# Performance work log

Hardware: AMD Instinct MI355X
Metric: run time of the kernel (lower is better)

## Reference

```python
import jax, jax.numpy as jnp
import numpy as np

V = 4          # view_num
B = 2048       # batch_size
D = 512        # feature dim
N = V * B
TEMP = 0.5     # temperature
EPS = 1e-8     # torch CosineSimilarity eps


def _neg_idx():
    # Row with residue p (position within its view block) masks out columns c
    # with c % B == p (the positive/self positions), exactly matching
    # mask_positive_samples: fill_diagonal_(0) on every BxB block.
    cols = np.arange(N)
    return np.stack([cols[cols % B != p] for p in range(B)])  # [B, N-V]

_NEG_IDX = jnp.asarray(_neg_idx())


def setup_inputs() -> dict:
    key = jax.random.key(0)
    x = jax.random.normal(key, (V, B, D), dtype=jnp.float32)
    return {"x": x}


def reference(x):
    # torch.cat(input, dim=0) -> [N, D]
    xf = x.reshape(N, D)
    # Cosine similarity via normalize + matmul (same math as broadcasted
    # CosineSimilarity(dim=2), expressed efficiently).
    norm = jnp.maximum(jnp.linalg.norm(xf, axis=1, keepdims=True), EPS)
    xn = xf / norm
    sim = (xn @ xn.T) / TEMP                                  # [N, N]

    # Negatives per anchor row: gather masked columns (same column order as
    # torch boolean-mask indexing, which is row-major ascending).
    sim_v = sim.reshape(V, B, N)
    negs = jnp.take_along_axis(sim_v, _NEG_IDX[None], axis=2)  # [V, B, N-V]
    lse_neg = jax.nn.logsumexp(negs, axis=2)                   # [V, B]

    # pos[i, j, b] = sim block-diagonal between views i and j
    pos = jnp.diagonal(sim.reshape(V, B, V, B), axis1=1, axis2=3)  # [V, V, B]

    # CrossEntropy with label 0 on logits = [pos_ij, negatives_i]:
    #   loss_b = logsumexp([pos, negs]) - pos = logaddexp(pos, lse_neg) - pos
    lse = jnp.logaddexp(pos, lse_neg[:, None, :])              # [V, V, B]
    per_pair = (lse - pos).sum(axis=2) / B                     # [V, V]

    off_diag = 1.0 - jnp.eye(V, dtype=per_pair.dtype)          # skip j == i
    return jnp.sum(per_pair * off_diag)
```

## Files before the change

kernel.cpp:

```cpp
#include <hip/hip_runtime.h>

#define NV 4
#define NB 2048
#define ND 512
#define NN 8192

typedef __bf16 bf16x8 __attribute__((ext_vector_type(8)));
typedef float floatx4 __attribute__((ext_vector_type(4)));

__global__ __launch_bounds__(256) void normalize_k(const float* __restrict__ x,
                                                   __bf16* __restrict__ xn,
                                                   float* __restrict__ sumexp,
                                                   float* __restrict__ out) {
  if (threadIdx.x < 4) sumexp[blockIdx.x * 4 + threadIdx.x] = 0.0f;
  if (blockIdx.x == 0 && threadIdx.x == 0) out[0] = 0.0f;

  const int row = blockIdx.x * 4 + (threadIdx.x >> 6);
  const int l = threadIdx.x & 63;
  const float4* xr = (const float4*)(x + (size_t)row * ND);
  float4 v0 = xr[l * 2 + 0];
  float4 v1 = xr[l * 2 + 1];
  float ss = v0.x * v0.x + v0.y * v0.y + v0.z * v0.z + v0.w * v0.w +
             v1.x * v1.x + v1.y * v1.y + v1.z * v1.z + v1.w * v1.w;
#pragma unroll
  for (int off = 32; off > 0; off >>= 1) ss += __shfl_xor(ss, off, 64);
  const float inv = 1.0f / fmaxf(sqrtf(ss), 1e-8f);
  bf16x8 o;
  o[0] = (__bf16)(v0.x * inv); o[1] = (__bf16)(v0.y * inv);
  o[2] = (__bf16)(v0.z * inv); o[3] = (__bf16)(v0.w * inv);
  o[4] = (__bf16)(v1.x * inv); o[5] = (__bf16)(v1.y * inv);
  o[6] = (__bf16)(v1.z * inv); o[7] = (__bf16)(v1.w * inv);
  *(bf16x8*)(xn + (size_t)row * ND + l * 8) = o;
}

__device__ __forceinline__ void gl_lds16(const void* g, void* l) {
  __builtin_amdgcn_global_load_lds(
      (const __attribute__((address_space(1))) void*)g,
      (__attribute__((address_space(3))) void*)l, 16, 0, 0);
}

__global__ __launch_bounds__(256, 4) void sim_k(const __bf16* __restrict__ xn,
                                                float* __restrict__ sumexp,
                                                float* __restrict__ pos) {
  __shared__ __bf16 As[128 * 32];
  __shared__ __bf16 Bs[128 * 32];
  const int tid = threadIdx.x;
  const int w = tid >> 6, l = tid & 63;
  const int m = l & 15, q = l >> 4;
  const int wr = w >> 1, wc = w & 1;

  const int bid = blockIdx.x;
  int rt = (int)((129.0f - sqrtf(16641.0f - 8.0f * (float)bid)) * 0.5f);
  rt = rt < 0 ? 0 : (rt > 63 ? 63 : rt);
  while (rt > 0 && (rt * 64 - rt * (rt - 1) / 2) > bid) --rt;
  while (rt < 63 && ((rt + 1) * 64 - (rt + 1) * rt / 2) <= bid) ++rt;
  const int ct = rt + (bid - (rt * 64 - rt * (rt - 1) / 2));
  const bool diag = (rt == ct);

  floatx4 acc[4][4] = {};

  const char* gA = (const char*)xn + (size_t)rt * 128 * (ND * 2);
  const char* gB = (const char*)xn + (size_t)ct * 128 * (ND * 2);
  char* lA = (char*)As;
  char* lB = (char*)Bs;

  const int row0 = tid >> 2;
  const int kb = (tid & 3) * 16;

  for (int kt = 0; kt < ND / 32; ++kt) {
    const int kbyte0 = kt * 64;
    {
      const char* ga0 = gA + (size_t)row0 * (ND * 2) + kbyte0 + kb;
      const char* gb0 = gB + (size_t)row0 * (ND * 2) + kbyte0 + kb;
      const char* ga1 = gA + (size_t)(row0 + 64) * (ND * 2) + kbyte0 + kb;
      const char* gb1 = gB + (size_t)(row0 + 64) * (ND * 2) + kbyte0 + kb;
      gl_lds16(ga0, lA + w * 1024);
      gl_lds16(gb0, lB + w * 1024);
      gl_lds16(ga1, lA + 4096 + w * 1024);
      gl_lds16(gb1, lB + 4096 + w * 1024);
    }
    __syncthreads();
    bf16x8 af[4], bfr[4];
#pragma unroll
    for (int mt = 0; mt < 4; ++mt)
      af[mt] = *(const bf16x8*)(lA + (wr * 64 + mt * 16 + m) * 64 + q * 16);
#pragma unroll
    for (int nt = 0; nt < 4; ++nt)
      bfr[nt] = *(const bf16x8*)(lB + (wc * 64 + nt * 16 + m) * 64 + q * 16);
#pragma unroll
    for (int mt = 0; mt < 4; ++mt)
#pragma unroll
      for (int nt = 0; nt < 4; ++nt)
        acc[mt][nt] = __builtin_amdgcn_mfma_f32_16x16x32_bf16(
            af[mt], bfr[nt], acc[mt][nt], 0, 0, 0);
    __syncthreads();
  }

  const int r0 = rt * 128 + wr * 64;
  const int c0 = ct * 128 + wc * 64;
  float cs[4] = {0.f, 0.f, 0.f, 0.f};
#pragma unroll
  for (int mt = 0; mt < 4; ++mt) {
    float rs[4] = {0.f, 0.f, 0.f, 0.f};
#pragma unroll
    for (int nt = 0; nt < 4; ++nt) {
      const int c = c0 + nt * 16 + m;
#pragma unroll
      for (int reg = 0; reg < 4; ++reg) {
        const int r = r0 + mt * 16 + q * 4 + reg;
        const float s = acc[mt][nt][reg] * 2.0f;
        if (((c - r) & (NB - 1)) == 0) {
          pos[r * NV + (c >> 11)] = s;
          if (!diag) pos[c * NV + (r >> 11)] = s;
        } else {
          const float e = __expf(s);
          rs[reg] += e;
          cs[nt] += e;
        }
      }
    }
#pragma unroll
    for (int off = 1; off < 16; off <<= 1) {
#pragma unroll
      for (int reg = 0; reg < 4; ++reg) rs[reg] += __shfl_xor(rs[reg], off, 64);
    }
    if (m < 4) atomicAdd(&sumexp[r0 + mt * 16 + q * 4 + m], rs[m]);
  }
  if (!diag) {
#pragma unroll
    for (int nt = 0; nt < 4; ++nt) {
      cs[nt] += __shfl_xor(cs[nt], 16, 64);
      cs[nt] += __shfl_xor(cs[nt], 32, 64);
    }
    if (q == 0) {
#pragma unroll
      for (int nt = 0; nt < 4; ++nt)
        atomicAdd(&sumexp[c0 + nt * 16 + m], cs[nt]);
    }
  }
}

__global__ __launch_bounds__(256) void finalize_k(
    const float* __restrict__ sumexp, const float* __restrict__ pos,
    float* __restrict__ out) {
  const int r = blockIdx.x * 256 + threadIdx.x;
  const float se = sumexp[r];
  const int i = r >> 11;
  float local = 0.0f;
#pragma unroll
  for (int j = 0; j < NV; ++j) {
    if (j == i) continue;
    const float p = pos[r * NV + j];
    local += logf(__expf(p) + se) - p;
  }
  local *= (1.0f / NB);
#pragma unroll
  for (int off = 32; off > 0; off >>= 1) local += __shfl_xor(local, off, 64);
  if ((threadIdx.x & 63) == 0) atomicAdd(out, local);
}

extern "C" void kernel_launch(void* const* d_in, const int* in_sizes, int n_in,
                              void* d_out, int out_size, void* d_ws,
                              size_t ws_size, hipStream_t stream) {
  const float* x = (const float*)d_in[0];
  float* out = (float*)d_out;
  char* ws = (char*)d_ws;
  __bf16* xn = (__bf16*)ws;
  float* sumexp = (float*)(ws + (size_t)NN * ND * 2);
  float* pos = (float*)(ws + (size_t)NN * ND * 2 + NN * 4);

  normalize_k<<<NN / 4, 256, 0, stream>>>(x, xn, sumexp, out);
  sim_k<<<64 * 65 / 2, 256, 0, stream>>>(xn, sumexp, pos);
  finalize_k<<<NN / 256, 256, 0, stream>>>(sumexp, pos, out);
}
```

Baseline: 120.2 us.

## Switch similarity GEMM to FP8 e4m3 with scaled MFMA and swizzled LDS tiles

Normalized features are now quantized to FP8 e4m3 instead of bf16, and the Gram matrix is computed with the MI355X scaled MFMA 16x16x128 f8f6f4 instruction using unit scales. K tiles grow to 128 bytes per row, with an XOR swizzle on the LDS layout to avoid bank conflicts and a fully unrolled 4-step K loop. This halves operand bytes and raises MFMA throughput per instruction, at the cost of lower precision in the similarity values that feed exp and logsumexp. LDS use grows, so occupancy drops to three blocks per CU.

```diff
diff --git a/kernel.cpp b/kernel.cpp
--- a/kernel.cpp
+++ b/kernel.cpp
@@ -1,15 +1,17 @@
 #include <hip/hip_runtime.h>
+#include <hip/hip_fp8.h>
 
 #define NV 4
 #define NB 2048
 #define ND 512
 #define NN 8192
 
-typedef __bf16 bf16x8 __attribute__((ext_vector_type(8)));
+typedef int int8v __attribute__((ext_vector_type(8)));
 typedef float floatx4 __attribute__((ext_vector_type(4)));
+#define SCALE1 0x7F7F7F7Fu
 
 __global__ __launch_bounds__(256) void normalize_k(const float* __restrict__ x,
-                                                   __bf16* __restrict__ xn,
+                                                   unsigned char* __restrict__ xn,
                                                    float* __restrict__ sumexp,
                                                    float* __restrict__ out) {
   if (threadIdx.x < 4) sumexp[blockIdx.x * 4 + threadIdx.x] = 0.0f;
@@ -25,12 +27,16 @@
 #pragma unroll
   for (int off = 32; off > 0; off >>= 1) ss += __shfl_xor(ss, off, 64);
   const float inv = 1.0f / fmaxf(sqrtf(ss), 1e-8f);
-  bf16x8 o;
-  o[0] = (__bf16)(v0.x * inv); o[1] = (__bf16)(v0.y * inv);
-  o[2] = (__bf16)(v0.z * inv); o[3] = (__bf16)(v0.w * inv);
-  o[4] = (__bf16)(v1.x * inv); o[5] = (__bf16)(v1.y * inv);
-  o[6] = (__bf16)(v1.z * inv); o[7] = (__bf16)(v1.w * inv);
-  *(bf16x8*)(xn + (size_t)row * ND + l * 8) = o;
+  union { unsigned char b[8]; uint2 u; } pk;
+  pk.b[0] = __hip_fp8_e4m3(v0.x * inv).__x;
+  pk.b[1] = __hip_fp8_e4m3(v0.y * inv).__x;
+  pk.b[2] = __hip_fp8_e4m3(v0.z * inv).__x;
+  pk.b[3] = __hip_fp8_e4m3(v0.w * inv).__x;
+  pk.b[4] = __hip_fp8_e4m3(v1.x * inv).__x;
+  pk.b[5] = __hip_fp8_e4m3(v1.y * inv).__x;
+  pk.b[6] = __hip_fp8_e4m3(v1.z * inv).__x;
+  pk.b[7] = __hip_fp8_e4m3(v1.w * inv).__x;
+  *(uint2*)(xn + (size_t)row * ND + l * 8) = pk.u;
 }
 
 __device__ __forceinline__ void gl_lds16(const void* g, void* l) {
@@ -39,14 +45,14 @@
       (__attribute__((address_space(3))) void*)l, 16, 0, 0);
 }
 
-__global__ __launch_bounds__(256, 4) void sim_k(const __bf16* __restrict__ xn,
+__global__ __launch_bounds__(256, 3) void sim_k(const unsigned char* __restrict__ xn,
                                                 float* __restrict__ sumexp,
                                                 float* __restrict__ pos) {
-  __shared__ __bf16 As[128 * 32];
-  __shared__ __bf16 Bs[128 * 32];
+  __shared__ unsigned char As[128 * 128];
+  __shared__ unsigned char Bs[128 * 128];
   const int tid = threadIdx.x;
   const int w = tid >> 6, l = tid & 63;
-  const int m = l & 15, q = l >> 4;
+  const int m = l & 15, q = l >> 4, s = l & 7;
   const int wr = w >> 1, wc = w & 1;
 
   const int bid = blockIdx.x;
@@ -59,40 +65,43 @@
 
   floatx4 acc[4][4] = {};
 
-  const char* gA = (const char*)xn + (size_t)rt * 128 * (ND * 2);
-  const char* gB = (const char*)xn + (size_t)ct * 128 * (ND * 2);
-  char* lA = (char*)As;
-  char* lB = (char*)Bs;
+  const unsigned char* gA = xn + (size_t)rt * 128 * ND;
+  const unsigned char* gB = xn + (size_t)ct * 128 * ND;
 
-  const int row0 = tid >> 2;
-  const int kb = (tid & 3) * 16;
+  const int rr = l >> 3;
+  const int swz = ((l & 7) ^ rr) * 16;
 
-  for (int kt = 0; kt < ND / 32; ++kt) {
-    const int kbyte0 = kt * 64;
-    {
-      const char* ga0 = gA + (size_t)row0 * (ND * 2) + kbyte0 + kb;
-      const char* gb0 = gB + (size_t)row0 * (ND * 2) + kbyte0 + kb;
-      const char* ga1 = gA + (size_t)(row0 + 64) * (ND * 2) + kbyte0 + kb;
-      const char* gb1 = gB + (size_t)(row0 + 64) * (ND * 2) + kbyte0 + kb;
-      gl_lds16(ga0, lA + w * 1024);
-      gl_lds16(gb0, lB + w * 1024);
-      gl_lds16(ga1, lA + 4096 + w * 1024);
-      gl_lds16(gb1, lB + 4096 + w * 1024);
+#pragma unroll
+  for (int kt = 0; kt < ND / 128; ++kt) {
+    const int kb0 = kt * 128;
+#pragma unroll
+    for (int i = 0; i < 4; ++i) {
+      const int v = i * 4 + w;
+      const size_t grow = (size_t)(v * 8 + rr) * ND + kb0 + swz;
+      gl_lds16(gA + grow, As + v * 1024);
+      gl_lds16(gB + grow, Bs + v * 1024);
     }
     __syncthreads();
-    bf16x8 af[4], bfr[4];
 #pragma unroll
-    for (int mt = 0; mt < 4; ++mt)
-      af[mt] = *(const bf16x8*)(lA + (wr * 64 + mt * 16 + m) * 64 + q * 16);
+    for (int mt = 0; mt < 4; ++mt) {
+      const unsigned char* pa = As + (wr * 64 + mt * 16 + m) * 128;
+      int4 alo = *(const int4*)(pa + (((2 * q + 0) ^ s) * 16));
+      int4 ahi = *(const int4*)(pa + (((2 * q + 1) ^ s) * 16));
+      int8v af;
+      af[0] = alo.x; af[1] = alo.y; af[2] = alo.z; af[3] = alo.w;
+      af[4] = ahi.x; af[5] = ahi.y; af[6] = ahi.z; af[7] = ahi.w;
 #pragma unroll
-    for (int nt = 0; nt < 4; ++nt)
-      bfr[nt] = *(const bf16x8*)(lB + (wc * 64 + nt * 16 + m) * 64 + q * 16);
-#pragma unroll
-    for (int mt = 0; mt < 4; ++mt)
-#pragma unroll
-      for (int nt = 0; nt < 4; ++nt)
-        acc[mt][nt] = __builtin_amdgcn_mfma_f32_16x16x32_bf16(
-            af[mt], bfr[nt], acc[mt][nt], 0, 0, 0);
+      for (int nt = 0; nt < 4; ++nt) {
+        const unsigned char* pb = Bs + (wc * 64 + nt * 16 + m) * 128;
+        int4 blo = *(const int4*)(pb + (((2 * q + 0) ^ s) * 16));
+        int4 bhi = *(const int4*)(pb + (((2 * q + 1) ^ s) * 16));
+        int8v bf;
+        bf[0] = blo.x; bf[1] = blo.y; bf[2] = blo.z; bf[3] = blo.w;
+        bf[4] = bhi.x; bf[5] = bhi.y; bf[6] = bhi.z; bf[7] = bhi.w;
+        acc[mt][nt] = __builtin_amdgcn_mfma_scale_f32_16x16x128_f8f6f4(
+            af, bf, acc[mt][nt], 0, 0, 0, SCALE1, 0, SCALE1);
+      }
+    }
     __syncthreads();
   }
 
@@ -108,12 +117,12 @@
 #pragma unroll
       for (int reg = 0; reg < 4; ++reg) {
         const int r = r0 + mt * 16 + q * 4 + reg;
-        const float s = acc[mt][nt][reg] * 2.0f;
+        const float sv = acc[mt][nt][reg] * 2.0f;
         if (((c - r) & (NB - 1)) == 0) {
-          pos[r * NV + (c >> 11)] = s;
-          if (!diag) pos[c * NV + (r >> 11)] = s;
+          pos[r * NV + (c >> 11)] = sv;
+          if (!diag) pos[c * NV + (r >> 11)] = sv;
         } else {
-          const float e = __expf(s);
+          const float e = __expf(sv);
           rs[reg] += e;
           cs[nt] += e;
         }
@@ -165,9 +174,9 @@
   const float* x = (const float*)d_in[0];
   float* out = (float*)d_out;
   char* ws = (char*)d_ws;
-  __bf16* xn = (__bf16*)ws;
-  float* sumexp = (float*)(ws + (size_t)NN * ND * 2);
-  float* pos = (float*)(ws + (size_t)NN * ND * 2 + NN * 4);
+  unsigned char* xn = (unsigned char*)ws;
+  float* sumexp = (float*)(ws + (size_t)NN * ND);
+  float* pos = (float*)(ws + (size_t)NN * ND + NN * 4);
 
   normalize_k<<<NN / 4, 256, 0, stream>>>(x, xn, sumexp, out);
   sim_k<<<64 * 65 / 2, 256, 0, stream>>>(xn, sumexp, pos);
```

Result: slower. 257.2 us (+114.0%).
